# Optimization experiments

Hardware: AMD Instinct MI355X
Metric: run time of the kernel (lower is better)

Reference implementation:

```python
import jax, jax.numpy as jnp
import numpy as np

N = 100000   # nodes
E = 1600000  # edges (avg degree 16)
H = 128      # hidden_channels
OUT = 64     # out_channels


def setup_inputs() -> dict:
    key = jax.random.key(0)
    ks = jax.random.split(key, 12)
    def lin(k, fan_in, fan_out):
        s = 1.0 / np.sqrt(fan_in)
        kw, kb = jax.random.split(k)
        W = jax.random.uniform(kw, (fan_in, fan_out), jnp.float32, -s, s)
        b = jax.random.uniform(kb, (fan_out,), jnp.float32, -s, s)
        return W, b
    W1, b1 = lin(ks[2], 1, H)
    W2, b2 = lin(ks[3], H, H)
    W3, b3 = lin(ks[4], H, H)
    Wo, bo = lin(ks[5], H, OUT)
    return {
        "x": jax.random.normal(ks[0], (N, 1), jnp.float32),
        "edge_index": jax.random.randint(ks[1], (2, E), 0, N, jnp.int32),
        "W1": W1, "b1": b1,
        "W2": W2, "b2": b2,
        "W3": W3, "b3": b3,
        "Wo": Wo, "bo": bo,
    }


def _gcn_conv(x, W, b, src, dst, dinv):
    # PyG GCNConv: x' = W x, then deg-normalized scatter-add over edges (+bias)
    h = x @ W                              # [N, C_out]
    norm = dinv[src] * dinv[dst]           # [E+N]
    msg = h[src] * norm[:, None]           # gather + scale  [E+N, C_out]
    out = jax.ops.segment_sum(msg, dst, num_segments=N)  # scatter-add
    return out + b


def reference(x, edge_index, W1, b1, W2, b2, W3, b3, Wo, bo):
    # add self-loops (GCNConv default add_self_loops=True)
    loop = jnp.arange(N, dtype=edge_index.dtype)
    src = jnp.concatenate([edge_index[0], loop])
    dst = jnp.concatenate([edge_index[1], loop])
    # symmetric normalization: deg over destination nodes, weight=1
    deg = jax.ops.segment_sum(jnp.ones_like(dst, jnp.float32), dst, num_segments=N)
    dinv = jnp.where(deg > 0, jax.lax.rsqrt(jnp.maximum(deg, 1.0)), 0.0)

    # layer 1: GCNConv -> dropout(eval=identity) -> relu
    h = jax.nn.relu(_gcn_conv(x, W1, b1, src, dst, dinv))
    # mid layer (num_layers=3 -> one mid block): GCNConv -> dropout -> relu
    h = jax.nn.relu(_gcn_conv(h, W2, b2, src, dst, dinv))
    # last layer: GCNConv -> dropout (no relu)
    h = _gcn_conv(h, W3, b3, src, dst, dinv)
    # linear head
    return h @ Wo + bo
```

## Files before the change

kernel.cpp:

```cpp
#include <hip/hip_runtime.h>

#define GN 100000
#define GE 1600000
#define GH 128
#define GOUT 64

#define NBUCK 98
#define BCAP 17664
#define P1B 98
#define P1E 16384

#define NPW 25
#define CAPE 480

typedef _Float16 half8v __attribute__((ext_vector_type(8)));
typedef _Float16 half4v __attribute__((ext_vector_type(4)));
typedef _Float16 half2v __attribute__((ext_vector_type(2)));
typedef float floatx4 __attribute__((ext_vector_type(4)));

__device__ __forceinline__ float dot2acc(half2v a, half2v b, float c) {
#if __has_builtin(__builtin_amdgcn_fdot2)
  return __builtin_amdgcn_fdot2(a, b, c, false);
#else
  return fmaf((float)a[0], (float)b[0], fmaf((float)a[1], (float)b[1], c));
#endif
}


__global__ __launch_bounds__(256) void k_prep(const float* __restrict__ W1, const float* __restrict__ b1,
                                              const float* __restrict__ W2, const float* __restrict__ W3,
                                              const float* __restrict__ Wo, const float* __restrict__ b3,
                                              const float* __restrict__ bo, unsigned* __restrict__ tabS,
                                              float* __restrict__ knots, _Float16* __restrict__ Wch,
                                              float* __restrict__ bch, int* __restrict__ rowStart,
                                              int* __restrict__ gCnt) {
  int tid = threadIdx.x;
  int blk = blockIdx.x;
  if (blk == 0) {
    __shared__ _Float16 sW2[GH * GH];
    __shared__ float sW1[GH], sb1[GH], th[GH];
    __shared__ int sidx[GH];
    for (int i = tid; i < GH * GH / 4; i += 256) {
      float4 v = ((const float4*)W2)[i];
      half4v h;
      h[0] = (_Float16)v.x; h[1] = (_Float16)v.y; h[2] = (_Float16)v.z; h[3] = (_Float16)v.w;
      ((half4v*)sW2)[i] = h;
    }
    if (tid < GH) {
      float w1 = W1[tid], bb = b1[tid];
      sW1[tid] = w1;
      sb1[tid] = bb;
      th[tid] = (w1 != 0.0f) ? (-bb / w1) : 3.0e38f;
    }
    __syncthreads();
    if (tid < GH) {
      float my = th[tid];
      int r = 0;
      for (int j = 0; j < GH; ++j) {
        float tj = th[j];
        r += (tj < my) || (tj == my && j < tid);
      }
      sidx[r] = tid;
      knots[r] = my;
    }
    __syncthreads();
    if (tid < GH) {
      int c = tid;
      float A = 0.f, B = 0.f;
      for (int k = 0; k < GH; ++k) {
        float w1 = sW1[k];
        float w2 = (float)sW2[k * GH + c];
        if (w1 < 0.0f) {
          A = fmaf(w1, w2, A);
          B = fmaf(sb1[k], w2, B);
        } else if (w1 == 0.0f && sb1[k] > 0.0f) {
          B = fmaf(sb1[k], w2, B);
        }
      }
      for (int b = 0; b <= GH; ++b) {
        half2v hh;
        hh[0] = (_Float16)A;
        hh[1] = (_Float16)B;
        tabS[((b * 64 + (c >> 1)) << 1) + (c & 1)] = __builtin_bit_cast(unsigned, hh);
        if (b < GH) {
          int k = sidx[b];
          float w1 = sW1[k];
          float w2 = (float)sW2[k * GH + c];
          if (w1 > 0.0f) {
            A = fmaf(w1, w2, A);
            B = fmaf(sb1[k], w2, B);
          } else if (w1 < 0.0f) {
            A = fmaf(-w1, w2, A);
            B = fmaf(-sb1[k], w2, B);
          }
        }
      }
    }
  } else if (blk <= 32) {
    int idx = (blk - 1) * 256 + tid;
    int k = idx >> 6, c = idx & 63;
    float s = 0.f;
#pragma unroll 8
    for (int j = 0; j < GH; ++j) s = fmaf(W3[k * GH + j], Wo[j * GOUT + c], s);
    Wch[idx] = (_Float16)s;
  } else {
    if (tid < GOUT) {
      float s = bo[tid];
      for (int j = 0; j < GH; ++j) s = fmaf(b3[j], Wo[j * GOUT + tid], s);
      bch[tid] = s;
    }
    if (tid >= 128 && tid < 128 + NBUCK) gCnt[tid - 128] = 0;
    if (tid == 255) rowStart[GN] = GE;
  }
}


__global__ __launch_bounds__(1024) void p1_fused(const int* __restrict__ ei, int* __restrict__ gCnt,
                                                 unsigned* __restrict__ staged) {
  __shared__ int cur[NBUCK];
  __shared__ int base[NBUCK];
  int tid = threadIdx.x, b = blockIdx.x;
  if (tid < NBUCK) cur[tid] = 0;
  __syncthreads();
  int e0 = b * P1E;
  int eend = e0 + P1E;
  if (eend > GE) eend = GE;
  for (int e = e0 + tid; e < eend; e += 1024) {
    int dst = ei[GE + e];
    atomicAdd(&cur[dst >> 10], 1);
  }
  __syncthreads();
  if (tid < NBUCK) {
    base[tid] = atomicAdd(&gCnt[tid], cur[tid]);
    cur[tid] = 0;
  }
  __syncthreads();
  for (int e = e0 + tid; e < eend; e += 1024) {
    int src = ei[e];
    int dst = ei[GE + e];
    int bb = dst >> 10;
    int r = atomicAdd(&cur[bb], 1);
    int pos = base[bb] + r;
    if (pos < BCAP) staged[(size_t)bb * BCAP + pos] = ((unsigned)src << 10) | (unsigned)(dst & 1023);
  }
}


__global__ __launch_bounds__(1024) void p2_build(const unsigned* __restrict__ staged,
                                                 const int* __restrict__ gCnt, const float* __restrict__ x,
                                                 float* __restrict__ dinv, float* __restrict__ xs,
                                                 int* __restrict__ rowStart, int* __restrict__ csr) {
  __shared__ int cntL[1024];
  __shared__ int curL[1024];
  __shared__ int wsum[16];
  __shared__ int totL[NBUCK];
  __shared__ int baseSh;
  int b = blockIdx.x;
  int tid = threadIdx.x;
  if (tid < NBUCK) totL[tid] = gCnt[tid];
  cntL[tid] = 0;
  __syncthreads();
  if (tid == 0) {
    int s = 0;
    for (int j = 0; j < b; ++j) s += totL[j];
    baseSh = s;
  }
  int n = totL[b];
  if (n > BCAP) n = BCAP;
  __syncthreads();
  int base = baseSh;
  const unsigned* st = staged + (size_t)b * BCAP;
  for (int i = tid; i < n; i += 1024) {
    unsigned u = st[i];
    atomicAdd(&cntL[u & 1023], 1);
  }
  __syncthreads();
  int v = cntL[tid];
  int lane = tid & 63, w = tid >> 6;
  int inc = v;
#pragma unroll
  for (int off = 1; off < 64; off <<= 1) {
    int u = __shfl_up(inc, off, 64);
    if (lane >= off) inc += u;
  }
  if (lane == 63) wsum[w] = inc;
  __syncthreads();
  int woff = 0;
  for (int i = 0; i < w; ++i) woff += wsum[i];
  int ex = inc - v + woff;
  int node = b * 1024 + tid;
  if (node < GN) {
    rowStart[node] = base + ex;
    float dv = rsqrtf((float)(v + 1));
    dinv[node] = dv;
    xs[node] = x[node] * dv;
  }
  curL[tid] = ex;
  __syncthreads();
  for (int i = tid; i < n; i += 1024) {
    unsigned u = st[i];
    int pos = atomicAdd(&curL[u & 1023], 1);
    csr[base + pos] = (int)(u >> 10);
  }
}


__global__ __launch_bounds__(256) void k_layer1(const float* __restrict__ xs, const int* __restrict__ rowStart,
                                                const int* __restrict__ csr, const float* __restrict__ dinv,
                                                const float* __restrict__ knots, uint2* __restrict__ pqb) {
  __shared__ float kn[GH];
  int tid = threadIdx.x;
  if (tid < GH) kn[tid] = knots[tid];
  __syncthreads();
  int d = blockIdx.x * 256 + tid;
  if (d >= GN) return;
  float acc = xs[d];
  int e = rowStart[d];
  int en = rowStart[d + 1];
  for (; e + 4 <= en; e += 4) {
    int s0 = csr[e], s1 = csr[e + 1], s2 = csr[e + 2], s3 = csr[e + 3];
    acc += xs[s0] + xs[s1] + xs[s2] + xs[s3];
  }
  for (; e < en; ++e) acc += xs[csr[e]];
  float q = dinv[d];
  float u = acc * q;
  int lo = 0;
#pragma unroll
  for (int s = 64; s > 0; s >>= 1)
    if (kn[lo + s - 1] < u) lo += s;
  if (lo < GH && kn[lo] < u) ++lo;
  half2v ph;
  ph[0] = (_Float16)(u * q);
  ph[1] = (_Float16)q;
  pqb[d] = make_uint2(__builtin_bit_cast(unsigned, ph), (unsigned)(lo << 9));
}


__global__ __launch_bounds__(1024) void k_exp_full(const uint2* __restrict__ pqb, const int* __restrict__ csr,
                                                   const int* __restrict__ rowStart, const unsigned* __restrict__ tabS,
                                                   const float* __restrict__ dinv, const float* __restrict__ b2,
                                                   _Float16* __restrict__ h2out) {
  __shared__ __align__(16) uint2 sTab[129 * 64];
  __shared__ __align__(16) uint2 sBuf[16 * CAPE];
  int tid = threadIdx.x;
  {
    const uint4* tg = (const uint4*)tabS;
    uint4* td = (uint4*)sTab;
    for (int i = tid; i < 4128; i += 1024) td[i] = tg[i];
  }
  int lane = tid & 63, wv = tid >> 6;
  int wid = blockIdx.x * 16 + wv;
  int n0 = wid * NPW;
  int rsv = rowStart[n0 + (lane <= NPW ? lane : NPW)];
  int eBeg = __builtin_amdgcn_readlane(rsv, 0);
  int eTot = __builtin_amdgcn_readlane(rsv, NPW) - eBeg;
  int nE = eTot < CAPE ? eTot : CAPE;
  int srcv[8];
#pragma unroll
  for (int c = 0; c < 8; ++c) {
    int i = c * 64 + lane;
    srcv[c] = csr[i < nE ? eBeg + i : eBeg];
  }
  uint2 pv[8];
#pragma unroll
  for (int c = 0; c < 8; ++c) pv[c] = pqb[srcv[c]];
  uint2* bw = sBuf + wv * CAPE;
#pragma unroll
  for (int c = 0; c < 8; ++c) {
    int i = c * 64 + lane;
    if (i < nE) bw[i] = pv[c];
  }
  __syncthreads();

  const char* tbl = (const char*)sTab + lane * 8;
  const char* bwB = (const char*)bw;
  float2 bb = ((const float2*)b2)[lane];

  uint2 selfv = pqb[n0];
  float dvv = dinv[n0];
  uint2 selfN = pqb[n0 + 1];
  float dvN = dinv[n0 + 1];

  float a0 = 0.f, a1 = 0.f;
  auto proc = [&](uint2 v) {
    uint2 t = *(const uint2*)(tbl + v.y);
    half2v ph = __builtin_bit_cast(half2v, v.x);
    a0 = dot2acc(__builtin_bit_cast(half2v, t.x), ph, a0);
    a1 = dot2acc(__builtin_bit_cast(half2v, t.y), ph, a1);
  };

  int sB = 0;
  for (int d = 0; d < NPW; ++d) {
    int sE = __builtin_amdgcn_readlane(rsv, d + 1) - eBeg;
    a0 = 0.f;
    a1 = 0.f;
    int lim = sE < nE ? sE : nE;
    int j = sB;
    for (; j + 4 <= lim; j += 4) {
      const char* p = bwB + (size_t)j * 8;
      uint2 v0 = *(const uint2*)(p);
      uint2 v1 = *(const uint2*)(p + 8);
      uint2 v2 = *(const uint2*)(p + 16);
      uint2 v3 = *(const uint2*)(p + 24);
      uint2 t0 = *(const uint2*)(tbl + v0.y);
      uint2 t1 = *(const uint2*)(tbl + v1.y);
      uint2 t2 = *(const uint2*)(tbl + v2.y);
      uint2 t3 = *(const uint2*)(tbl + v3.y);
      half2v p0 = __builtin_bit_cast(half2v, v0.x);
      half2v p1 = __builtin_bit_cast(half2v, v1.x);
      half2v p2 = __builtin_bit_cast(half2v, v2.x);
      half2v p3 = __builtin_bit_cast(half2v, v3.x);
      a0 = dot2acc(__builtin_bit_cast(half2v, t0.x), p0, a0);
      a1 = dot2acc(__builtin_bit_cast(half2v, t0.y), p0, a1);
      a0 = dot2acc(__builtin_bit_cast(half2v, t1.x), p1, a0);
      a1 = dot2acc(__builtin_bit_cast(half2v, t1.y), p1, a1);
      a0 = dot2acc(__builtin_bit_cast(half2v, t2.x), p2, a0);
      a1 = dot2acc(__builtin_bit_cast(half2v, t2.y), p2, a1);
      a0 = dot2acc(__builtin_bit_cast(half2v, t3.x), p3, a0);
      a1 = dot2acc(__builtin_bit_cast(half2v, t3.y), p3, a1);
    }
    for (; j < lim; ++j) proc(*(const uint2*)(bwB + (size_t)j * 8));
    for (int j2 = (sB > nE ? sB : nE); j2 < sE; ++j2) {
      int s2 = csr[eBeg + j2];
      proc(pqb[s2]);
    }
    proc(selfv);
    float r0 = fmaxf(fmaf(a0, dvv, bb.x), 0.f);
    float r1 = fmaxf(fmaf(a1, dvv, bb.y), 0.f);
    half2v o;
    o[0] = (_Float16)r0;
    o[1] = (_Float16)r1;
    ((unsigned*)h2out)[(size_t)(n0 + d) * 64 + lane] = __builtin_bit_cast(unsigned, o);
    selfv = selfN;
    dvv = dvN;
    if (d + 2 < NPW) {
      selfN = pqb[n0 + d + 2];
      dvN = dinv[n0 + d + 2];
    }
    sB = sE;
  }
}


template <int NCOL>
__global__ __launch_bounds__(256) void gemm_f16k(const _Float16* __restrict__ A, const _Float16* __restrict__ Wh,
                                                 const float* __restrict__ dinv, _Float16* __restrict__ Cout,
                                                 int ntiles) {
  constexpr int NT = NCOL / 16;
  constexpr int WS = 136;
  __shared__ __align__(16) _Float16 WtL[NCOL * WS];
  int tid = threadIdx.x;
  for (int i = tid; i < GH * NCOL; i += 256) {
    int k = i / NCOL, n = i % NCOL;
    WtL[n * WS + k] = Wh[i];
  }
  __syncthreads();
  int lane = tid & 63;
  int waveId = tid >> 6;
  int m = lane & 15, q = lane >> 4;

  for (int t = blockIdx.x * 4 + waveId; t < ntiles; t += gridDim.x * 4) {
    int row = t * 16 + m;
    const _Float16* arow = A + (size_t)row * GH + q * 8;
    half8v af[4];
#pragma unroll
    for (int ks = 0; ks < 4; ++ks) af[ks] = *(const half8v*)(arow + ks * 32);
    floatx4 acc[NT];
#pragma unroll
    for (int nt = 0; nt < NT; ++nt) {
      floatx4 z = {0.0f, 0.0f, 0.0f, 0.0f};
      acc[nt] = z;
    }
#pragma unroll
    for (int ks = 0; ks < 4; ++ks) {
#pragma unroll
      for (int nt = 0; nt < NT; ++nt) {
        half8v wf = *(const half8v*)(&WtL[(nt * 16 + m) * WS + ks * 32 + q * 8]);
        acc[nt] = __builtin_amdgcn_mfma_f32_16x16x32_f16(wf, af[ks], acc[nt], 0, 0, 0);
      }
    }
    float sc = dinv[row];
    _Float16* crow = Cout + (size_t)row * NCOL;
#pragma unroll
    for (int nt = 0; nt < NT; ++nt) {
      half4v h;
#pragma unroll
      for (int j = 0; j < 4; ++j) h[j] = (_Float16)(acc[nt][j] * sc);
      *(half4v*)(crow + nt * 16 + q * 4) = h;
    }
  }
}


__global__ __launch_bounds__(256) void k_agg64(const _Float16* __restrict__ ht, const int* __restrict__ rowStart,
                                               const int* __restrict__ csr, const float* __restrict__ dinv,
                                               const float* __restrict__ bias, float* __restrict__ out) {
  int gt = blockIdx.x * 256 + threadIdx.x;
  int wave = gt >> 6;
  int lane = threadIdx.x & 63;
  int half = lane >> 5;
  int l = lane & 31;
  int d = wave * 2 + half;
  if (d >= GN) return;
  const unsigned* htu = (const unsigned*)ht;
  half2v sv = __builtin_bit_cast(half2v, htu[(size_t)d * 32 + l]);
  float a0 = (float)sv[0], a1 = (float)sv[1];
  int e = rowStart[d];
  int en = rowStart[d + 1];
  unsigned rA0, rA1, rA2, rA3, rB0, rB1, rB2, rB3;
  bool hA = (e + 4 <= en);
  if (hA) {
    int s0 = csr[e], s1 = csr[e + 1], s2 = csr[e + 2], s3 = csr[e + 3];
    rA0 = htu[(size_t)s0 * 32 + l]; rA1 = htu[(size_t)s1 * 32 + l];
    rA2 = htu[(size_t)s2 * 32 + l]; rA3 = htu[(size_t)s3 * 32 + l];
  }
  bool hB = (e + 8 <= en);
  if (hB) {
    int s0 = csr[e + 4], s1 = csr[e + 5], s2 = csr[e + 6], s3 = csr[e + 7];
    rB0 = htu[(size_t)s0 * 32 + l]; rB1 = htu[(size_t)s1 * 32 + l];
    rB2 = htu[(size_t)s2 * 32 + l]; rB3 = htu[(size_t)s3 * 32 + l];
  }
  while (hA) {
    bool hC = (e + 12 <= en);
    unsigned rC0, rC1, rC2, rC3;
    if (hC) {
      int n0 = csr[e + 8], n1 = csr[e + 9], n2 = csr[e + 10], n3 = csr[e + 11];
      rC0 = htu[(size_t)n0 * 32 + l]; rC1 = htu[(size_t)n1 * 32 + l];
      rC2 = htu[(size_t)n2 * 32 + l]; rC3 = htu[(size_t)n3 * 32 + l];
    }
    half2v v0 = __builtin_bit_cast(half2v, rA0), v1 = __builtin_bit_cast(half2v, rA1);
    half2v v2 = __builtin_bit_cast(half2v, rA2), v3 = __builtin_bit_cast(half2v, rA3);
    a0 += (float)v0[0] + (float)v1[0] + (float)v2[0] + (float)v3[0];
    a1 += (float)v0[1] + (float)v1[1] + (float)v2[1] + (float)v3[1];
    rA0 = rB0; rA1 = rB1; rA2 = rB2; rA3 = rB3;
    rB0 = rC0; rB1 = rC1; rB2 = rC2; rB3 = rC3;
    e += 4;
    hA = hB;
    hB = hC;
  }
  for (; e < en; ++e) {
    half2v v = __builtin_bit_cast(half2v, htu[(size_t)csr[e] * 32 + l]);
    a0 += (float)v[0];
    a1 += (float)v[1];
  }
  float dv = dinv[d];
  float2 bb = ((const float2*)bias)[l];
  float2 o;
  o.x = fmaf(a0, dv, bb.x);
  o.y = fmaf(a1, dv, bb.y);
  ((float2*)out)[(size_t)d * 32 + l] = o;
}


extern "C" void kernel_launch(void* const* d_in, const int* in_sizes, int n_in,
                              void* d_out, int out_size, void* d_ws, size_t ws_size,
                              hipStream_t stream) {
  const float* x  = (const float*)d_in[0];
  const int*   ei = (const int*)d_in[1];
  const float* W1 = (const float*)d_in[2];
  const float* b1 = (const float*)d_in[3];
  const float* W2 = (const float*)d_in[4];
  const float* b2 = (const float*)d_in[5];
  const float* W3 = (const float*)d_in[6];
  const float* b3 = (const float*)d_in[7];
  const float* Wo = (const float*)d_in[8];
  const float* bo = (const float*)d_in[9];
  float* out = (float*)d_out;

  char* ws = (char*)d_ws;
  size_t off = 0;
  auto alloc = [&](size_t bytes) -> char* {
    off = (off + 255) & ~(size_t)255;
    char* p = ws + off;
    off += bytes;
    return p;
  };
  float*     dinv      = (float*)alloc((size_t)GN * 4);
  float*     xs        = (float*)alloc((size_t)GN * 4);
  int*       rowStart  = (int*)alloc((size_t)(GN + 1) * 4);
  int*       gCnt      = (int*)alloc((size_t)128 * 4);
  int*       csr       = (int*)alloc((size_t)GE * 4);
  unsigned*  tabS      = (unsigned*)alloc((size_t)129 * 128 * 4);
  float*     knots     = (float*)alloc((size_t)GH * 4);
  _Float16*  Wch       = (_Float16*)alloc((size_t)GH * GOUT * 2);
  float*     bch       = (float*)alloc((size_t)GOUT * 4);
  uint2*     pqb       = (uint2*)alloc((size_t)GN * 8);
  _Float16*  bufA      = (_Float16*)alloc((size_t)GN * GH * 2);
  _Float16*  bufB      = (_Float16*)alloc((size_t)GN * GOUT * 2);
  unsigned*  staged    = (unsigned*)bufA;
  (void)ws_size; (void)in_sizes; (void)n_in; (void)out_size;

  const int NTILES = GN / 16;
  const int GEMM_GRID = 782;

  k_prep<<<34, 256, 0, stream>>>(W1, b1, W2, W3, Wo, b3, bo, tabS, knots, Wch, bch, rowStart, gCnt);

  p1_fused<<<P1B, 1024, 0, stream>>>(ei, gCnt, staged);
  p2_build<<<NBUCK, 1024, 0, stream>>>(staged, gCnt, x, dinv, xs, rowStart, csr);

  k_layer1<<<(GN + 255) / 256, 256, 0, stream>>>(xs, rowStart, csr, dinv, knots, pqb);

  k_exp_full<<<250, 1024, 0, stream>>>(pqb, csr, rowStart, tabS, dinv, b2, bufA);

  gemm_f16k<GOUT><<<GEMM_GRID, 256, 0, stream>>>(bufA, Wch, dinv, bufB, NTILES);
  k_agg64<<<(GN / 2 + 3) / 4, 256, 0, stream>>>(bufB, rowStart, csr, dinv, bch, out);
}
```

Before: 263.3 us.

## Fuse layer-1 aggregation into CSR scatter, register-stage edges, split accumulators

```diff
diff --git a/kernel.cpp b/kernel.cpp
--- a/kernel.cpp
+++ b/kernel.cpp
@@ -123,11 +123,21 @@
   if (tid < NBUCK) cur[tid] = 0;
   __syncthreads();
   int e0 = b * P1E;
-  int eend = e0 + P1E;
-  if (eend > GE) eend = GE;
-  for (int e = e0 + tid; e < eend; e += 1024) {
-    int dst = ei[GE + e];
-    atomicAdd(&cur[dst >> 10], 1);
+  int sv[16], dv[16];
+#pragma unroll
+  for (int k = 0; k < 16; ++k) {
+    int e = e0 + k * 1024 + tid;
+    if (e < GE) {
+      sv[k] = ei[e];
+      dv[k] = ei[GE + e];
+    } else {
+      sv[k] = 0;
+      dv[k] = -1;
+    }
+  }
+#pragma unroll
+  for (int k = 0; k < 16; ++k) {
+    if (dv[k] >= 0) atomicAdd(&cur[dv[k] >> 10], 1);
   }
   __syncthreads();
   if (tid < NBUCK) {
@@ -135,23 +145,23 @@
     cur[tid] = 0;
   }
   __syncthreads();
-  for (int e = e0 + tid; e < eend; e += 1024) {
-    int src = ei[e];
-    int dst = ei[GE + e];
-    int bb = dst >> 10;
-    int r = atomicAdd(&cur[bb], 1);
-    int pos = base[bb] + r;
-    if (pos < BCAP) staged[(size_t)bb * BCAP + pos] = ((unsigned)src << 10) | (unsigned)(dst & 1023);
-  }
-}
-
-
-__global__ __launch_bounds__(1024) void p2_build(const unsigned* __restrict__ staged,
-                                                 const int* __restrict__ gCnt, const float* __restrict__ x,
-                                                 float* __restrict__ dinv, float* __restrict__ xs,
-                                                 int* __restrict__ rowStart, int* __restrict__ csr) {
+#pragma unroll
+  for (int k = 0; k < 16; ++k) {
+    if (dv[k] >= 0) {
+      int bb = dv[k] >> 10;
+      int r = atomicAdd(&cur[bb], 1);
+      int pos = base[bb] + r;
+      if (pos < BCAP) staged[(size_t)bb * BCAP + pos] = ((unsigned)sv[k] << 10) | (unsigned)(dv[k] & 1023);
+    }
+  }
+}
+
+
+__global__ __launch_bounds__(1024) void p2a_build(const unsigned* __restrict__ staged,
+                                                  const int* __restrict__ gCnt, const float* __restrict__ x,
+                                                  float* __restrict__ dinv, float* __restrict__ xs,
+                                                  int* __restrict__ rowStart) {
   __shared__ int cntL[1024];
-  __shared__ int curL[1024];
   __shared__ int wsum[16];
   __shared__ int totL[NBUCK];
   __shared__ int baseSh;
@@ -170,10 +180,7 @@
   __syncthreads();
   int base = baseSh;
   const unsigned* st = staged + (size_t)b * BCAP;
-  for (int i = tid; i < n; i += 1024) {
-    unsigned u = st[i];
-    atomicAdd(&cntL[u & 1023], 1);
-  }
+  for (int i = tid; i < n; i += 1024) atomicAdd(&cntL[st[i] & 1023], 1);
   __syncthreads();
   int v = cntL[tid];
   int lane = tid & 63, w = tid >> 6;
@@ -195,44 +202,66 @@
     dinv[node] = dv;
     xs[node] = x[node] * dv;
   }
-  curL[tid] = ex;
-  __syncthreads();
-  for (int i = tid; i < n; i += 1024) {
-    unsigned u = st[i];
-    int pos = atomicAdd(&curL[u & 1023], 1);
-    csr[base + pos] = (int)(u >> 10);
-  }
-}
-
-
-__global__ __launch_bounds__(256) void k_layer1(const float* __restrict__ xs, const int* __restrict__ rowStart,
-                                                const int* __restrict__ csr, const float* __restrict__ dinv,
-                                                const float* __restrict__ knots, uint2* __restrict__ pqb) {
+}
+
+
+__global__ __launch_bounds__(1024) void p2b_scatter(const unsigned* __restrict__ staged,
+                                                    const int* __restrict__ gCnt, const float* __restrict__ xs,
+                                                    const float* __restrict__ dinv, const int* __restrict__ rowStart,
+                                                    const float* __restrict__ knots, int* __restrict__ csr,
+                                                    uint2* __restrict__ pqb) {
+  __shared__ int curL[1024];
+  __shared__ float accL[1024];
   __shared__ float kn[GH];
+  int b = blockIdx.x;
   int tid = threadIdx.x;
   if (tid < GH) kn[tid] = knots[tid];
-  __syncthreads();
-  int d = blockIdx.x * 256 + tid;
-  if (d >= GN) return;
-  float acc = xs[d];
-  int e = rowStart[d];
-  int en = rowStart[d + 1];
-  for (; e + 4 <= en; e += 4) {
-    int s0 = csr[e], s1 = csr[e + 1], s2 = csr[e + 2], s3 = csr[e + 3];
-    acc += xs[s0] + xs[s1] + xs[s2] + xs[s3];
-  }
-  for (; e < en; ++e) acc += xs[csr[e]];
-  float q = dinv[d];
-  float u = acc * q;
-  int lo = 0;
-#pragma unroll
-  for (int s = 64; s > 0; s >>= 1)
-    if (kn[lo + s - 1] < u) lo += s;
-  if (lo < GH && kn[lo] < u) ++lo;
-  half2v ph;
-  ph[0] = (_Float16)(u * q);
-  ph[1] = (_Float16)q;
-  pqb[d] = make_uint2(__builtin_bit_cast(unsigned, ph), (unsigned)(lo << 9));
+  int base = rowStart[b << 10];
+  int node = (b << 10) + tid;
+  curL[tid] = (node < GN) ? (rowStart[node] - base) : 0;
+  accL[tid] = 0.f;
+  int n = gCnt[b];
+  if (n > BCAP) n = BCAP;
+  __syncthreads();
+  const unsigned* st = staged + (size_t)b * BCAP;
+  int i = tid;
+  for (; i + 3072 < n; i += 4096) {
+    unsigned u0 = st[i], u1 = st[i + 1024], u2 = st[i + 2048], u3 = st[i + 3072];
+    float x0 = xs[u0 >> 10], x1 = xs[u1 >> 10], x2 = xs[u2 >> 10], x3 = xs[u3 >> 10];
+    int p0 = atomicAdd(&curL[u0 & 1023], 1);
+    csr[base + p0] = (int)(u0 >> 10);
+    atomicAdd(&accL[u0 & 1023], x0);
+    int p1 = atomicAdd(&curL[u1 & 1023], 1);
+    csr[base + p1] = (int)(u1 >> 10);
+    atomicAdd(&accL[u1 & 1023], x1);
+    int p2 = atomicAdd(&curL[u2 & 1023], 1);
+    csr[base + p2] = (int)(u2 >> 10);
+    atomicAdd(&accL[u2 & 1023], x2);
+    int p3 = atomicAdd(&curL[u3 & 1023], 1);
+    csr[base + p3] = (int)(u3 >> 10);
+    atomicAdd(&accL[u3 & 1023], x3);
+  }
+  for (; i < n; i += 1024) {
+    unsigned u = st[i];
+    float xv = xs[u >> 10];
+    int p = atomicAdd(&curL[u & 1023], 1);
+    csr[base + p] = (int)(u >> 10);
+    atomicAdd(&accL[u & 1023], xv);
+  }
+  __syncthreads();
+  if (node < GN) {
+    float q = dinv[node];
+    float u = (accL[tid] + xs[node]) * q;
+    int lo = 0;
+#pragma unroll
+    for (int s = 64; s > 0; s >>= 1)
+      if (kn[lo + s - 1] < u) lo += s;
+    if (lo < GH && kn[lo] < u) ++lo;
+    half2v ph;
+    ph[0] = (_Float16)(u * q);
+    ph[1] = (_Float16)q;
+    pqb[node] = make_uint2(__builtin_bit_cast(unsigned, ph), (unsigned)(lo << 9));
+  }
 }
 
 
@@ -294,8 +323,52 @@
     int sE = __builtin_amdgcn_readlane(rsv, d + 1) - eBeg;
     a0 = 0.f;
     a1 = 0.f;
+    float a2 = 0.f, a3 = 0.f;
     int lim = sE < nE ? sE : nE;
     int j = sB;
+    for (; j + 8 <= lim; j += 8) {
+      const char* p = bwB + (size_t)j * 8;
+      uint2 v0 = *(const uint2*)(p);
+      uint2 v1 = *(const uint2*)(p + 8);
+      uint2 v2 = *(const uint2*)(p + 16);
+      uint2 v3 = *(const uint2*)(p + 24);
+      uint2 v4 = *(const uint2*)(p + 32);
+      uint2 v5 = *(const uint2*)(p + 40);
+      uint2 v6 = *(const uint2*)(p + 48);
+      uint2 v7 = *(const uint2*)(p + 56);
+      uint2 t0 = *(const uint2*)(tbl + v0.y);
+      uint2 t1 = *(const uint2*)(tbl + v1.y);
+      uint2 t2 = *(const uint2*)(tbl + v2.y);
+      uint2 t3 = *(const uint2*)(tbl + v3.y);
+      uint2 t4 = *(const uint2*)(tbl + v4.y);
+      uint2 t5 = *(const uint2*)(tbl + v5.y);
+      uint2 t6 = *(const uint2*)(tbl + v6.y);
+      uint2 t7 = *(const uint2*)(tbl + v7.y);
+      half2v p0 = __builtin_bit_cast(half2v, v0.x);
+      half2v p1 = __builtin_bit_cast(half2v, v1.x);
+      half2v p2 = __builtin_bit_cast(half2v, v2.x);
+      half2v p3 = __builtin_bit_cast(half2v, v3.x);
+      half2v p4 = __builtin_bit_cast(half2v, v4.x);
+      half2v p5 = __builtin_bit_cast(half2v, v5.x);
+      half2v p6 = __builtin_bit_cast(half2v, v6.x);
+      half2v p7 = __builtin_bit_cast(half2v, v7.x);
+      a0 = dot2acc(__builtin_bit_cast(half2v, t0.x), p0, a0);
+      a1 = dot2acc(__builtin_bit_cast(half2v, t0.y), p0, a1);
+      a2 = dot2acc(__builtin_bit_cast(half2v, t1.x), p1, a2);
+      a3 = dot2acc(__builtin_bit_cast(half2v, t1.y), p1, a3);
+      a0 = dot2acc(__builtin_bit_cast(half2v, t2.x), p2, a0);
+      a1 = dot2acc(__builtin_bit_cast(half2v, t2.y), p2, a1);
+      a2 = dot2acc(__builtin_bit_cast(half2v, t3.x), p3, a2);
+      a3 = dot2acc(__builtin_bit_cast(half2v, t3.y), p3, a3);
+      a0 = dot2acc(__builtin_bit_cast(half2v, t4.x), p4, a0);
+      a1 = dot2acc(__builtin_bit_cast(half2v, t4.y), p4, a1);
+      a2 = dot2acc(__builtin_bit_cast(half2v, t5.x), p5, a2);
+      a3 = dot2acc(__builtin_bit_cast(half2v, t5.y), p5, a3);
+      a0 = dot2acc(__builtin_bit_cast(half2v, t6.x), p6, a0);
+      a1 = dot2acc(__builtin_bit_cast(half2v, t6.y), p6, a1);
+      a2 = dot2acc(__builtin_bit_cast(half2v, t7.x), p7, a2);
+      a3 = dot2acc(__builtin_bit_cast(half2v, t7.y), p7, a3);
+    }
     for (; j + 4 <= lim; j += 4) {
       const char* p = bwB + (size_t)j * 8;
       uint2 v0 = *(const uint2*)(p);
@@ -312,13 +385,15 @@
       half2v p3 = __builtin_bit_cast(half2v, v3.x);
       a0 = dot2acc(__builtin_bit_cast(half2v, t0.x), p0, a0);
       a1 = dot2acc(__builtin_bit_cast(half2v, t0.y), p0, a1);
-      a0 = dot2acc(__builtin_bit_cast(half2v, t1.x), p1, a0);
-      a1 = dot2acc(__builtin_bit_cast(half2v, t1.y), p1, a1);
+      a2 = dot2acc(__builtin_bit_cast(half2v, t1.x), p1, a2);
+      a3 = dot2acc(__builtin_bit_cast(half2v, t1.y), p1, a3);
       a0 = dot2acc(__builtin_bit_cast(half2v, t2.x), p2, a0);
       a1 = dot2acc(__builtin_bit_cast(half2v, t2.y), p2, a1);
-      a0 = dot2acc(__builtin_bit_cast(half2v, t3.x), p3, a0);
-      a1 = dot2acc(__builtin_bit_cast(half2v, t3.y), p3, a1);
-    }
+      a2 = dot2acc(__builtin_bit_cast(half2v, t3.x), p3, a2);
+      a3 = dot2acc(__builtin_bit_cast(half2v, t3.y), p3, a3);
+    }
+    a0 += a2;
+    a1 += a3;
     for (; j < lim; ++j) proc(*(const uint2*)(bwB + (size_t)j * 8));
     for (int j2 = (sB > nE ? sB : nE); j2 < sE; ++j2) {
       int s2 = csr[eBeg + j2];
@@ -496,9 +571,8 @@
   k_prep<<<34, 256, 0, stream>>>(W1, b1, W2, W3, Wo, b3, bo, tabS, knots, Wch, bch, rowStart, gCnt);
 
   p1_fused<<<P1B, 1024, 0, stream>>>(ei, gCnt, staged);
-  p2_build<<<NBUCK, 1024, 0, stream>>>(staged, gCnt, x, dinv, xs, rowStart, csr);
-
-  k_layer1<<<(GN + 255) / 256, 256, 0, stream>>>(xs, rowStart, csr, dinv, knots, pqb);
+  p2a_build<<<NBUCK, 1024, 0, stream>>>(staged, gCnt, x, dinv, xs, rowStart);
+  p2b_scatter<<<NBUCK, 1024, 0, stream>>>(staged, gCnt, xs, dinv, rowStart, knots, csr, pqb);
 
   k_exp_full<<<250, 1024, 0, stream>>>(pqb, csr, rowStart, tabS, dinv, b2, bufA);
 
```

Result: no change. 260.4 us (-1.1%).
